# Performance work log

Measured on AMD Instinct MI355X. Metric: run time of the kernel, lower is better.

Reference implementation:

```python
import jax, jax.numpy as jnp
import numpy as np
from jax import lax

N, H, BS = 256, 1024, 128
ALPHA, BETA, SIGMA = 60.0, 20.0, 5.0
EPS = 1e-8


def _mlp_w(key, n_in, n_out):
    return jax.random.normal(key, (n_out, n_in), dtype=jnp.float32) / np.sqrt(n_in)


def setup_inputs() -> dict:
    key = jax.random.key(0)
    ks = jax.random.split(key, 8)
    inp = {
        "t": jnp.zeros((), dtype=jnp.float32),
        "x": jax.random.normal(ks[0], (BS, N), dtype=jnp.float32),
        "Wf1": _mlp_w(ks[1], N, H), "bf1": jnp.zeros((H,), jnp.float32),
        "Wf2": _mlp_w(ks[2], H, N), "bf2": jnp.zeros((N,), jnp.float32),
        "Wg1": _mlp_w(ks[3], N, H), "bg1": jnp.zeros((H,), jnp.float32),
        "Wg2": _mlp_w(ks[4], H, N), "bg2": jnp.zeros((N,), jnp.float32),
        "Wk1": _mlp_w(ks[5], N, H), "bk1": jnp.zeros((H,), jnp.float32),
        "Wk2": _mlp_w(ks[6], H, N), "bk2": jnp.zeros((N,), jnp.float32),
    }
    return inp


def reference(t, x, Wf1, bf1, Wf2, bf2, Wg1, bg1, Wg2, bg2, Wk1, bk1, Wk2, bk2):
    def mlp(u, W1, b1, W2, b2):
        return jnp.tanh(u @ W1.T + b1) @ W2.T + b2

    def k_func(u):
        return mlp(u, Wk1, bk1, Wk2, bk2)

    f_out = mlp(x, Wf1, bf1, Wf2, bf2)          # f_model(t, x); t unused
    k_out = k_func(x)
    G_k_out = mlp(x, Wg1, bg1, Wg2, bg2)        # g_fn(x)[0]
    dx_dt = f_out + G_k_out

    # compute_k_jacobian: torch detaches u, so no grad flows to x here.
    # torch layout: J[b, j, i] = d k_i / d u_j  (transpose of jacfwd output)
    x_d = lax.stop_gradient(x)
    J_fwd = jax.vmap(jax.jacfwd(k_func))(x_d)   # [bs, i_out, j_in]
    J_x = jnp.swapaxes(J_fwd, 1, 2)             # [bs, j, i]

    k_norm = jnp.linalg.norm(k_out, axis=1)                      # [bs]
    Jf = jnp.einsum('bji,bi->bj', J_x, f_out)                    # bmm(J, f)
    Jf_norm = jnp.linalg.norm(Jf, axis=1)
    c1 = Jf_norm - ALPHA * k_norm ** (2 * SIGMA - 1)
    JG = jnp.einsum('bji,bi->bj', J_x, G_k_out)                  # bmm(J, G)
    c2 = jnp.sum(k_out * JG, axis=1) - BETA * k_norm ** (2 * SIGMA)

    mask = (c1 > EPS) | (c2 < -EPS)                              # [bs]
    dx_upd = jnp.where(mask[:, None], jnp.zeros_like(dx_dt), dx_dt)
    return (dx_upd + dx_dt) / 2
```

## Files before the change

kernel.cpp:

```cpp
#include <hip/hip_runtime.h>
#include <stdint.h>

#define N_ 256
#define H_ 1024
#define BS_ 128

#define WS_T     0
#define WS_SK    393216
#define WS_OACC  524288
#define WS_OPART 622592
#define WS_JPART 2195456
#define WS_FLOATS 3244032

__global__ __launch_bounds__(256) void k1_layer1(
    const float* __restrict__ x,
    const float* __restrict__ Wf1, const float* __restrict__ bf1,
    const float* __restrict__ Wg1, const float* __restrict__ bg1,
    const float* __restrict__ Wk1, const float* __restrict__ bk1,
    float* __restrict__ T, float* __restrict__ sk)
{
    const int bx = blockIdx.x;
    const int m  = bx >> 8;
    const int ht = (bx >> 4) & 15;
    const int rt = bx & 15;
    const int t  = threadIdx.x;
    const int h0 = ht * 64;
    const int r0 = rt * 8;

    const float* W  = (m == 0) ? Wf1 : (m == 1) ? Wg1 : Wk1;
    const float* b1 = (m == 0) ? bf1 : (m == 1) ? bg1 : bk1;

    __shared__ float xs[8][256];
    for (int u = t; u < 2048; u += 256)
        xs[u >> 8][u & 255] = x[(r0 + (u >> 8)) * N_ + (u & 255)];
    __syncthreads();

    const int hl = t & 63;
    const int rl = (t >> 6) * 2;
    const int h  = h0 + hl;

    float a0 = b1[h], a1 = a0;
    const float4* w4  = (const float4*)(W + h * N_);
    const float4* xa4 = (const float4*)xs[rl];
    const float4* xb4 = (const float4*)xs[rl + 1];
    #pragma unroll 8
    for (int c = 0; c < 64; ++c) {
        float4 w = w4[c];
        float4 a = xa4[c];
        float4 b = xb4[c];
        a0 += w.x * a.x + w.y * a.y + w.z * a.z + w.w * a.w;
        a1 += w.x * b.x + w.y * b.y + w.z * b.z + w.w * b.w;
    }
    const float v0 = tanhf(a0), v1 = tanhf(a1);
    T[(m * BS_ + r0 + rl) * H_ + h]     = v0;
    T[(m * BS_ + r0 + rl + 1) * H_ + h] = v1;
    if (m == 2) {
        sk[(r0 + rl) * H_ + h]     = 1.0f - v0 * v0;
        sk[(r0 + rl + 1) * H_ + h] = 1.0f - v1 * v1;
    }
}

__global__ __launch_bounds__(256) void k2_layer2(
    const float* __restrict__ T,
    const float* __restrict__ Wf2, const float* __restrict__ bf2,
    const float* __restrict__ Wg2, const float* __restrict__ bg2,
    const float* __restrict__ Wk2, const float* __restrict__ bk2,
    float* __restrict__ opart)
{
    const int bx = blockIdx.x;
    const int m  = bx >> 8;
    const int rt = (bx >> 4) & 15;
    const int ks = bx & 15;
    const int t  = threadIdx.x;
    const int r0 = rt * 8;
    const int k0 = ks * 64;

    const float* W  = (m == 0) ? Wf2 : (m == 1) ? Wg2 : Wk2;
    const float* b2 = (m == 0) ? bf2 : (m == 1) ? bg2 : bk2;

    __shared__ float ts[8][64];
    for (int u = t; u < 512; u += 256)
        ts[u >> 6][u & 63] = T[(m * BS_ + r0 + (u >> 6)) * H_ + k0 + (u & 63)];
    __syncthreads();

    float acc[8];
    const float bv = (ks == 0) ? b2[t] : 0.0f;
    #pragma unroll
    for (int r = 0; r < 8; ++r) acc[r] = bv;

    const float4* w4 = (const float4*)(W + t * H_ + k0);
    #pragma unroll 4
    for (int c = 0; c < 16; ++c) {
        float4 w = w4[c];
        #pragma unroll
        for (int r = 0; r < 8; ++r) {
            float4 a = ((const float4*)ts[r])[c];
            acc[r] += w.x * a.x + w.y * a.y + w.z * a.z + w.w * a.w;
        }
    }
    #pragma unroll
    for (int r = 0; r < 8; ++r)
        opart[((ks * 3 + m) * BS_ + r0 + r) * N_ + t] = acc[r];
}

__global__ __launch_bounds__(256) void k25_reduce(
    const float* __restrict__ opart, float* __restrict__ oacc)
{
    const int tid = blockIdx.x * 256 + threadIdx.x;
    float s = 0.f;
    #pragma unroll
    for (int ks = 0; ks < 16; ++ks)
        s += opart[ks * (3 * BS_ * N_) + tid];
    oacc[tid] = s;
}

__global__ __launch_bounds__(256) void k3_vj(
    const float* __restrict__ Wk1, const float* __restrict__ Wk2,
    const float* __restrict__ oacc, const float* __restrict__ sk,
    float* __restrict__ jpart)
{
    const int rp = blockIdx.x >> 4;
    const int q  = blockIdx.x & 15;
    const int t  = threadIdx.x;
    const int r0 = rp * 4;
    const int h0 = q * 64;

    __shared__ float fos[4][256], gos[4][256];
    __shared__ float sfv[4][64], sgv[4][64];
    for (int u = t; u < 1024; u += 256) {
        const int r = u >> 8, i = u & 255;
        fos[r][i] = oacc[(r0 + r) * N_ + i];
        gos[r][i] = oacc[(BS_ + r0 + r) * N_ + i];
    }
    __syncthreads();

    {
        const int hl = t & 63;
        const int rl = t >> 6;
        const int h  = h0 + hl;
        float vf = 0.f, vg = 0.f;
        const float* w2 = Wk2 + h;
        #pragma unroll 8
        for (int i = 0; i < 256; ++i) {
            const float wv = w2[i * H_];
            vf += wv * fos[rl][i];
            vg += wv * gos[rl][i];
        }
        const float s = sk[(r0 + rl) * H_ + h];
        sfv[rl][hl] = s * vf;
        sgv[rl][hl] = s * vg;
    }
    __syncthreads();

    {
        float jf[4] = {0.f, 0.f, 0.f, 0.f};
        float jg[4] = {0.f, 0.f, 0.f, 0.f};
        const float* w1 = Wk1 + h0 * N_ + t;
        #pragma unroll 8
        for (int hh = 0; hh < 64; ++hh) {
            const float wv = w1[hh * N_];
            #pragma unroll
            for (int r = 0; r < 4; ++r) {
                jf[r] += sfv[r][hh] * wv;
                jg[r] += sgv[r][hh] * wv;
            }
        }
        #pragma unroll
        for (int r = 0; r < 4; ++r) {
            jpart[((q * 2 + 0) * BS_ + r0 + r) * N_ + t] = jf[r];
            jpart[((q * 2 + 1) * BS_ + r0 + r) * N_ + t] = jg[r];
        }
    }
}

__global__ __launch_bounds__(256) void k4_final(
    const float* __restrict__ oacc,
    const float* __restrict__ jpart,
    float* __restrict__ out)
{
    const int r = blockIdx.x;
    const int t = threadIdx.x;
    __shared__ float red[12];

    const float fo = oacc[r * N_ + t];
    const float go = oacc[(BS_ + r) * N_ + t];
    const float ko = oacc[(2 * BS_ + r) * N_ + t];

    float jf = 0.f, jg = 0.f;
    #pragma unroll
    for (int q = 0; q < 16; ++q) {
        jf += jpart[((q * 2 + 0) * BS_ + r) * N_ + t];
        jg += jpart[((q * 2 + 1) * BS_ + r) * N_ + t];
    }

    float v0 = ko * ko, v1 = jf * jf, v2 = ko * jg;
    #pragma unroll
    for (int o = 32; o > 0; o >>= 1) {
        v0 += __shfl_xor(v0, o, 64);
        v1 += __shfl_xor(v1, o, 64);
        v2 += __shfl_xor(v2, o, 64);
    }
    const int wid = t >> 6;
    if ((t & 63) == 0) {
        red[wid * 3 + 0] = v0;
        red[wid * 3 + 1] = v1;
        red[wid * 3 + 2] = v2;
    }
    __syncthreads();
    const float kn2 = red[0] + red[3] + red[6] + red[9];
    const float jf2 = red[1] + red[4] + red[7] + red[10];
    const float kjg = red[2] + red[5] + red[8] + red[11];

    const float knorm = sqrtf(kn2);
    const float kn4 = kn2 * kn2;
    const float kn8 = kn4 * kn4;
    const float c1 = sqrtf(jf2) - 60.0f * kn8 * knorm;
    const float c2 = kjg - 20.0f * kn8 * kn2;
    const float scale = ((c1 > 1e-8f) || (c2 < -1e-8f)) ? 0.5f : 1.0f;

    out[r * N_ + t] = (fo + go) * scale;
}

__global__ __launch_bounds__(256) void manifold_fused(
    const float* __restrict__ x,
    const float* __restrict__ Wf1, const float* __restrict__ bf1v,
    const float* __restrict__ Wf2, const float* __restrict__ bf2v,
    const float* __restrict__ Wg1, const float* __restrict__ bg1v,
    const float* __restrict__ Wg2, const float* __restrict__ bg2v,
    const float* __restrict__ Wk1, const float* __restrict__ bk1v,
    const float* __restrict__ Wk2, const float* __restrict__ bk2v,
    float* __restrict__ out)
{
    const int b = blockIdx.x;
    const int t = threadIdx.x;
    __shared__ float xs[N_];
    __shared__ float tf[H_], tg[H_], tk[H_], sk[H_];
    __shared__ float fo[N_], go[N_];
    __shared__ float sfv[H_], sgv[H_];
    __shared__ float red[12];

    xs[t] = x[b * N_ + t];
    __syncthreads();
    {
        float acc[12];
        const float4* rows[12];
        #pragma unroll
        for (int m = 0; m < 4; ++m) {
            const int h = t + m * 256;
            rows[m]     = (const float4*)(Wf1 + h * N_);
            rows[4 + m] = (const float4*)(Wg1 + h * N_);
            rows[8 + m] = (const float4*)(Wk1 + h * N_);
            acc[m] = bf1v[h]; acc[4 + m] = bg1v[h]; acc[8 + m] = bk1v[h];
        }
        const float4* xs4 = (const float4*)xs;
        #pragma unroll 2
        for (int c = 0; c < 64; ++c) {
            float4 a = xs4[c];
            #pragma unroll
            for (int r = 0; r < 12; ++r) {
                float4 w = rows[r][c];
                acc[r] += w.x * a.x + w.y * a.y + w.z * a.z + w.w * a.w;
            }
        }
        #pragma unroll
        for (int m = 0; m < 4; ++m) {
            const int h = t + m * 256;
            float vtf = tanhf(acc[m]);
            float vtg = tanhf(acc[4 + m]);
            float vtk = tanhf(acc[8 + m]);
            tf[h] = vtf; tg[h] = vtg; tk[h] = vtk; sk[h] = 1.0f - vtk * vtk;
        }
    }
    __syncthreads();
    float af = bf2v[t], ag = bg2v[t], ak = bk2v[t];
    {
        const float4* rf = (const float4*)(Wf2 + t * H_);
        const float4* rg = (const float4*)(Wg2 + t * H_);
        const float4* rk = (const float4*)(Wk2 + t * H_);
        #pragma unroll 2
        for (int c = 0; c < 256; ++c) {
            float4 wf = rf[c], wg = rg[c], wk = rk[c];
            float4 vf = ((const float4*)tf)[c];
            af += wf.x*vf.x + wf.y*vf.y + wf.z*vf.z + wf.w*vf.w;
            float4 vg = ((const float4*)tg)[c];
            ag += wg.x*vg.x + wg.y*vg.y + wg.z*vg.z + wg.w*vg.w;
            float4 vk = ((const float4*)tk)[c];
            ak += wk.x*vk.x + wk.y*vk.y + wk.z*vk.z + wk.w*vk.w;
        }
    }
    fo[t] = af; go[t] = ag;
    __syncthreads();
    {
        float vf[4] = {0.f,0.f,0.f,0.f}, vg[4] = {0.f,0.f,0.f,0.f};
        const float* base = Wk2 + 4 * t;
        #pragma unroll 4
        for (int i = 0; i < N_; ++i) {
            float4 w = *(const float4*)(base + i * H_);
            float fv = fo[i], gv = go[i];
            vf[0]+=w.x*fv; vf[1]+=w.y*fv; vf[2]+=w.z*fv; vf[3]+=w.w*fv;
            vg[0]+=w.x*gv; vg[1]+=w.y*gv; vg[2]+=w.z*gv; vg[3]+=w.w*gv;
        }
        #pragma unroll
        for (int c = 0; c < 4; ++c) {
            sfv[4*t+c] = sk[4*t+c]*vf[c];
            sgv[4*t+c] = sk[4*t+c]*vg[c];
        }
    }
    __syncthreads();
    float jf = 0.f, jg = 0.f;
    {
        const float* col = Wk1 + t;
        #pragma unroll 4
        for (int c = 0; c < 256; ++c) {
            float4 s4 = ((const float4*)sfv)[c];
            float4 g4 = ((const float4*)sgv)[c];
            const int h = c * 4;
            float w0 = col[(h+0)*N_], w1 = col[(h+1)*N_];
            float w2 = col[(h+2)*N_], w3 = col[(h+3)*N_];
            jf += s4.x*w0 + s4.y*w1 + s4.z*w2 + s4.w*w3;
            jg += g4.x*w0 + g4.y*w1 + g4.z*w2 + g4.w*w3;
        }
    }
    float v0 = ak*ak, v1 = jf*jf, v2 = ak*jg;
    #pragma unroll
    for (int o = 32; o > 0; o >>= 1) {
        v0 += __shfl_xor(v0, o, 64);
        v1 += __shfl_xor(v1, o, 64);
        v2 += __shfl_xor(v2, o, 64);
    }
    const int wid = t >> 6;
    if ((t & 63) == 0) {
        red[wid*3+0] = v0; red[wid*3+1] = v1; red[wid*3+2] = v2;
    }
    __syncthreads();
    const float kn2 = red[0]+red[3]+red[6]+red[9];
    const float jf2 = red[1]+red[4]+red[7]+red[10];
    const float kjg = red[2]+red[5]+red[8]+red[11];
    const float knorm = sqrtf(kn2);
    const float kn4 = kn2*kn2, kn8 = kn4*kn4;
    const float c1 = sqrtf(jf2) - 60.0f*kn8*knorm;
    const float c2 = kjg - 20.0f*kn8*kn2;
    const float scale = ((c1 > 1e-8f) || (c2 < -1e-8f)) ? 0.5f : 1.0f;
    out[b*N_+t] = (af+ag)*scale;
}

extern "C" void kernel_launch(void* const* d_in, const int* in_sizes, int n_in,
                              void* d_out, int out_size, void* d_ws, size_t ws_size,
                              hipStream_t stream) {
    const float* x    = (const float*)d_in[1];
    const float* Wf1  = (const float*)d_in[2];
    const float* bf1v = (const float*)d_in[3];
    const float* Wf2  = (const float*)d_in[4];
    const float* bf2v = (const float*)d_in[5];
    const float* Wg1  = (const float*)d_in[6];
    const float* bg1v = (const float*)d_in[7];
    const float* Wg2  = (const float*)d_in[8];
    const float* bg2v = (const float*)d_in[9];
    const float* Wk1  = (const float*)d_in[10];
    const float* bk1v = (const float*)d_in[11];
    const float* Wk2  = (const float*)d_in[12];
    const float* bk2v = (const float*)d_in[13];
    float* out = (float*)d_out;

    if (ws_size < (size_t)WS_FLOATS * sizeof(float)) {
        manifold_fused<<<BS_, 256, 0, stream>>>(
            x, Wf1, bf1v, Wf2, bf2v, Wg1, bg1v, Wg2, bg2v,
            Wk1, bk1v, Wk2, bk2v, out);
        return;
    }

    float* ws    = (float*)d_ws;
    float* T     = ws + WS_T;
    float* sk    = ws + WS_SK;
    float* oacc  = ws + WS_OACC;
    float* opart = ws + WS_OPART;
    float* jpart = ws + WS_JPART;

    k1_layer1 <<<768, 256, 0, stream>>>(x, Wf1, bf1v, Wg1, bg1v, Wk1, bk1v, T, sk);
    k2_layer2 <<<768, 256, 0, stream>>>(T, Wf2, bf2v, Wg2, bg2v, Wk2, bk2v, opart);
    k25_reduce<<<384, 256, 0, stream>>>(opart, oacc);
    k3_vj     <<<512, 256, 0, stream>>>(Wk1, Wk2, oacc, sk, jpart);
    k4_final  <<<BS_, 256, 0, stream>>>(oacc, jpart, out);
}
```

Before: 136.0 us.

## Fuse layer-1 and layer-2 kernels via shared-memory hidden tile; vectorize VJ loops

Merges the layer-1 tanh kernel and the layer-2 split-K kernel into one launch. Each block now keeps its 8x64 hidden-activation tile in shared memory and immediately computes the matching layer-2 partial products, so the T buffer is never written to or read back from global memory. The VJ kernel also drops its shared-memory staging of f/g outputs in favour of wave-uniform float4 reads, and reads the sfv/sgv values as float4. This saves one kernel launch and the global round-trip of the hidden activations, at the cost of higher per-block shared-memory use and register pressure.

After: 135.7 us. Within noise of the previous version (-0.2%).

```diff
diff --git a/kernel.cpp b/kernel.cpp
--- a/kernel.cpp
+++ b/kernel.cpp
@@ -5,19 +5,21 @@
 #define H_ 1024
 #define BS_ 128
 
-#define WS_T     0
-#define WS_SK    393216
-#define WS_OACC  524288
-#define WS_OPART 622592
-#define WS_JPART 2195456
-#define WS_FLOATS 3244032
-
-__global__ __launch_bounds__(256) void k1_layer1(
+#define WS_SK    0
+#define WS_OACC  131072
+#define WS_OPART 229376
+#define WS_JPART 1802240
+#define WS_FLOATS 2850816
+
+__global__ __launch_bounds__(256) void k12_l1l2(
     const float* __restrict__ x,
     const float* __restrict__ Wf1, const float* __restrict__ bf1,
     const float* __restrict__ Wg1, const float* __restrict__ bg1,
     const float* __restrict__ Wk1, const float* __restrict__ bk1,
-    float* __restrict__ T, float* __restrict__ sk)
+    const float* __restrict__ Wf2, const float* __restrict__ bf2,
+    const float* __restrict__ Wg2, const float* __restrict__ bg2,
+    const float* __restrict__ Wk2, const float* __restrict__ bk2,
+    float* __restrict__ sk, float* __restrict__ opart)
 {
     const int bx = blockIdx.x;
     const int m  = bx >> 8;
@@ -27,80 +29,63 @@
     const int h0 = ht * 64;
     const int r0 = rt * 8;
 
-    const float* W  = (m == 0) ? Wf1 : (m == 1) ? Wg1 : Wk1;
+    const float* W1 = (m == 0) ? Wf1 : (m == 1) ? Wg1 : Wk1;
     const float* b1 = (m == 0) ? bf1 : (m == 1) ? bg1 : bk1;
+    const float* W2 = (m == 0) ? Wf2 : (m == 1) ? Wg2 : Wk2;
+    const float* b2 = (m == 0) ? bf2 : (m == 1) ? bg2 : bk2;
 
     __shared__ float xs[8][256];
+    __shared__ float ts[8][64];
     for (int u = t; u < 2048; u += 256)
         xs[u >> 8][u & 255] = x[(r0 + (u >> 8)) * N_ + (u & 255)];
     __syncthreads();
 
-    const int hl = t & 63;
-    const int rl = (t >> 6) * 2;
-    const int h  = h0 + hl;
-
-    float a0 = b1[h], a1 = a0;
-    const float4* w4  = (const float4*)(W + h * N_);
-    const float4* xa4 = (const float4*)xs[rl];
-    const float4* xb4 = (const float4*)xs[rl + 1];
-    #pragma unroll 8
-    for (int c = 0; c < 64; ++c) {
-        float4 w = w4[c];
-        float4 a = xa4[c];
-        float4 b = xb4[c];
-        a0 += w.x * a.x + w.y * a.y + w.z * a.z + w.w * a.w;
-        a1 += w.x * b.x + w.y * b.y + w.z * b.z + w.w * b.w;
-    }
-    const float v0 = tanhf(a0), v1 = tanhf(a1);
-    T[(m * BS_ + r0 + rl) * H_ + h]     = v0;
-    T[(m * BS_ + r0 + rl + 1) * H_ + h] = v1;
-    if (m == 2) {
-        sk[(r0 + rl) * H_ + h]     = 1.0f - v0 * v0;
-        sk[(r0 + rl + 1) * H_ + h] = 1.0f - v1 * v1;
-    }
-}
-
-__global__ __launch_bounds__(256) void k2_layer2(
-    const float* __restrict__ T,
-    const float* __restrict__ Wf2, const float* __restrict__ bf2,
-    const float* __restrict__ Wg2, const float* __restrict__ bg2,
-    const float* __restrict__ Wk2, const float* __restrict__ bk2,
-    float* __restrict__ opart)
-{
-    const int bx = blockIdx.x;
-    const int m  = bx >> 8;
-    const int rt = (bx >> 4) & 15;
-    const int ks = bx & 15;
-    const int t  = threadIdx.x;
-    const int r0 = rt * 8;
-    const int k0 = ks * 64;
-
-    const float* W  = (m == 0) ? Wf2 : (m == 1) ? Wg2 : Wk2;
-    const float* b2 = (m == 0) ? bf2 : (m == 1) ? bg2 : bk2;
-
-    __shared__ float ts[8][64];
-    for (int u = t; u < 512; u += 256)
-        ts[u >> 6][u & 63] = T[(m * BS_ + r0 + (u >> 6)) * H_ + k0 + (u & 63)];
-    __syncthreads();
-
-    float acc[8];
-    const float bv = (ks == 0) ? b2[t] : 0.0f;
-    #pragma unroll
-    for (int r = 0; r < 8; ++r) acc[r] = bv;
-
-    const float4* w4 = (const float4*)(W + t * H_ + k0);
-    #pragma unroll 4
-    for (int c = 0; c < 16; ++c) {
-        float4 w = w4[c];
-        #pragma unroll
-        for (int r = 0; r < 8; ++r) {
-            float4 a = ((const float4*)ts[r])[c];
-            acc[r] += w.x * a.x + w.y * a.y + w.z * a.z + w.w * a.w;
-        }
-    }
-    #pragma unroll
-    for (int r = 0; r < 8; ++r)
-        opart[((ks * 3 + m) * BS_ + r0 + r) * N_ + t] = acc[r];
+    {
+        const int hl = t & 63;
+        const int rg = (t >> 6) * 2;
+        const int h  = h0 + hl;
+        float a0 = b1[h], a1 = a0;
+        const float4* w4  = (const float4*)(W1 + h * N_);
+        const float4* xa4 = (const float4*)xs[rg];
+        const float4* xb4 = (const float4*)xs[rg + 1];
+        #pragma unroll 8
+        for (int c = 0; c < 64; ++c) {
+            float4 w = w4[c];
+            float4 a = xa4[c];
+            float4 b = xb4[c];
+            a0 += w.x * a.x + w.y * a.y + w.z * a.z + w.w * a.w;
+            a1 += w.x * b.x + w.y * b.y + w.z * b.z + w.w * b.w;
+        }
+        const float v0 = tanhf(a0), v1 = tanhf(a1);
+        ts[rg][hl]     = v0;
+        ts[rg + 1][hl] = v1;
+        if (m == 2) {
+            sk[(r0 + rg) * H_ + h]     = 1.0f - v0 * v0;
+            sk[(r0 + rg + 1) * H_ + h] = 1.0f - v1 * v1;
+        }
+    }
+    __syncthreads();
+
+    {
+        float acc[8];
+        const float bv = (ht == 0) ? b2[t] : 0.0f;
+        #pragma unroll
+        for (int r = 0; r < 8; ++r) acc[r] = bv;
+
+        const float4* w4 = (const float4*)(W2 + t * H_ + h0);
+        #pragma unroll 4
+        for (int c = 0; c < 16; ++c) {
+            float4 w = w4[c];
+            #pragma unroll
+            for (int r = 0; r < 8; ++r) {
+                float4 a = ((const float4*)ts[r])[c];
+                acc[r] += w.x * a.x + w.y * a.y + w.z * a.z + w.w * a.w;
+            }
+        }
+        #pragma unroll
+        for (int r = 0; r < 8; ++r)
+            opart[((ht * 3 + m) * BS_ + r0 + r) * N_ + t] = acc[r];
+    }
 }
 
 __global__ __launch_bounds__(256) void k25_reduce(
@@ -125,26 +110,26 @@
     const int r0 = rp * 4;
     const int h0 = q * 64;
 
-    __shared__ float fos[4][256], gos[4][256];
     __shared__ float sfv[4][64], sgv[4][64];
-    for (int u = t; u < 1024; u += 256) {
-        const int r = u >> 8, i = u & 255;
-        fos[r][i] = oacc[(r0 + r) * N_ + i];
-        gos[r][i] = oacc[(BS_ + r0 + r) * N_ + i];
-    }
-    __syncthreads();
 
     {
         const int hl = t & 63;
-        const int rl = t >> 6;
+        const int rl = __builtin_amdgcn_readfirstlane(t >> 6);
         const int h  = h0 + hl;
+        const float* fo_p = oacc + (r0 + rl) * N_;
+        const float* go_p = oacc + (BS_ + r0 + rl) * N_;
+        const float* w2   = Wk2 + h;
         float vf = 0.f, vg = 0.f;
-        const float* w2 = Wk2 + h;
         #pragma unroll 8
-        for (int i = 0; i < 256; ++i) {
-            const float wv = w2[i * H_];
-            vf += wv * fos[rl][i];
-            vg += wv * gos[rl][i];
+        for (int c = 0; c < 64; ++c) {
+            const float4 of = *(const float4*)(fo_p + 4 * c);
+            const float4 og = *(const float4*)(go_p + 4 * c);
+            const float w0 = w2[(4 * c + 0) * H_];
+            const float w1 = w2[(4 * c + 1) * H_];
+            const float w2v = w2[(4 * c + 2) * H_];
+            const float w3 = w2[(4 * c + 3) * H_];
+            vf += of.x * w0 + of.y * w1 + of.z * w2v + of.w * w3;
+            vg += og.x * w0 + og.y * w1 + og.z * w2v + og.w * w3;
         }
         const float s = sk[(r0 + rl) * H_ + h];
         sfv[rl][hl] = s * vf;
@@ -156,13 +141,18 @@
         float jf[4] = {0.f, 0.f, 0.f, 0.f};
         float jg[4] = {0.f, 0.f, 0.f, 0.f};
         const float* w1 = Wk1 + h0 * N_ + t;
-        #pragma unroll 8
-        for (int hh = 0; hh < 64; ++hh) {
-            const float wv = w1[hh * N_];
+        #pragma unroll 4
+        for (int c = 0; c < 16; ++c) {
+            const float w0 = w1[(4 * c + 0) * N_];
+            const float wv1 = w1[(4 * c + 1) * N_];
+            const float wv2 = w1[(4 * c + 2) * N_];
+            const float wv3 = w1[(4 * c + 3) * N_];
             #pragma unroll
             for (int r = 0; r < 4; ++r) {
-                jf[r] += sfv[r][hh] * wv;
-                jg[r] += sgv[r][hh] * wv;
+                const float4 sf = ((const float4*)sfv[r])[c];
+                const float4 sg = ((const float4*)sgv[r])[c];
+                jf[r] += sf.x * w0 + sf.y * wv1 + sf.z * wv2 + sf.w * wv3;
+                jg[r] += sg.x * w0 + sg.y * wv1 + sg.z * wv2 + sg.w * wv3;
             }
         }
         #pragma unroll
@@ -370,14 +360,14 @@
     }
 
     float* ws    = (float*)d_ws;
-    float* T     = ws + WS_T;
     float* sk    = ws + WS_SK;
     float* oacc  = ws + WS_OACC;
     float* opart = ws + WS_OPART;
     float* jpart = ws + WS_JPART;
 
-    k1_layer1 <<<768, 256, 0, stream>>>(x, Wf1, bf1v, Wg1, bg1v, Wk1, bk1v, T, sk);
-    k2_layer2 <<<768, 256, 0, stream>>>(T, Wf2, bf2v, Wg2, bg2v, Wk2, bk2v, opart);
+    k12_l1l2  <<<768, 256, 0, stream>>>(x, Wf1, bf1v, Wg1, bg1v, Wk1, bk1v,
+                                        Wf2, bf2v, Wg2, bg2v, Wk2, bk2v,
+                                        sk, opart);
     k25_reduce<<<384, 256, 0, stream>>>(opart, oacc);
     k3_vj     <<<512, 256, 0, stream>>>(Wk1, Wk2, oacc, sk, jpart);
     k4_final  <<<BS_, 256, 0, stream>>>(oacc, jpart, out);
```
